# Kernel tuning notes

Hardware: AMD Instinct MI355X
Metric: run time of the kernel (lower is better)

## Reference

```python
import jax, jax.numpy as jnp
import numpy as np

B, S, D, H = 2, 2048, 1024, 16
DH = D // H  # 64


def setup_inputs() -> dict:
    key = jax.random.key(0)
    k1, k2, k3, k4 = jax.random.split(key, 4)
    x = jax.random.normal(k1, (B, S, D), dtype=jnp.float32)
    # causal mask: 0 => masked (matches mask==0 -> -inf in source)
    mask = jnp.tril(jnp.ones((S, S), dtype=jnp.int32))
    Wq = jax.random.normal(k2, (H, D, DH), dtype=jnp.float32) * (D ** -0.5)
    Wk = jax.random.normal(k3, (H, D, DH), dtype=jnp.float32) * (D ** -0.5)
    Wo = jax.random.normal(k4, (D, D), dtype=jnp.float32) * (D ** -0.5)
    bo = jnp.zeros((D,), dtype=jnp.float32)
    return {"x": x, "mask": mask, "Wq": Wq, "Wk": Wk, "Wo": Wo, "bo": bo}


def reference(x, mask, Wq, Wk, Wo, bo):
    # Per source: q = query(x), k = key(x), v = query(x)  (bug kept: v == q)
    q = jnp.einsum('bsd,hde->bhse', x, Wq)   # [B,H,S,DH]
    k = jnp.einsum('bsd,hde->bhse', x, Wk)   # [B,H,S,DH]
    # scale uses d_model (input dim), not d_head -- faithful to source
    scale = jnp.asarray(D, x.dtype) ** -0.5
    scores = jnp.einsum('bhse,bhte->bhst', q, k) * scale  # [B,H,S,S]
    neg_inf = jnp.asarray(float('-inf'), scores.dtype)
    scores = jnp.where(mask[None, None, :, :] == 0, neg_inf, scores)
    w = jax.nn.softmax(scores, axis=-1)
    attn = jnp.einsum('bhst,bhte->bhse', w, q)  # v == q
    # concat heads: head axis becomes contiguous feature blocks
    attn = attn.transpose(0, 2, 1, 3).reshape(B, S, D)
    return attn @ Wo + bo
```

## Files before the change

### kernel.cpp

```cpp
#include <hip/hip_runtime.h>
#include <hip/hip_bf16.h>

#define BQ 2
#define SQ 2048
#define DMODEL 1024
#define NH 16
#define DH 64
#define NQT (SQ / 64)

typedef __attribute__((ext_vector_type(8))) short bf16x8;
typedef __attribute__((ext_vector_type(4))) short bf16x4;
typedef __attribute__((ext_vector_type(4))) float f32x4;
typedef unsigned short u16;

__device__ __forceinline__ u16 f2b(float f) {
  __hip_bfloat16 h = __float2bfloat16(f);
  return *reinterpret_cast<u16*>(&h);
}

#define MFMA(a, b, c) __builtin_amdgcn_mfma_f32_16x16x32_bf16((a), (b), (c), 0, 0, 0)

__device__ __forceinline__ f32x4 mfma16(bf16x4 a, bf16x4 b, f32x4 c) {
  asm("v_mfma_f32_16x16x16_bf16 %0, %1, %2, %0" : "+v"(c) : "v"(a), "v"(b));
  return c;
}

__device__ __forceinline__ unsigned cvtpk(float lo, float hi) {
  unsigned r;
  asm("v_cvt_pk_bf16_f32 %0, %1, %2" : "=v"(r) : "v"(lo), "v"(hi));
  return r;
}

#define CS (0.03125f * 1.44269504088896f)


__global__ void cvt_x_kernel(const float* __restrict__ x, u16* __restrict__ xb, int n) {
  int i = blockIdx.x * blockDim.x + threadIdx.x;
  int stride = gridDim.x * blockDim.x;
  for (; i < n; i += stride) xb[i] = f2b(x[i]);
}

__global__ void transpose_head_kernel(const float* __restrict__ W, u16* __restrict__ WT) {
  int i = blockIdx.x * blockDim.x + threadIdx.x;
  const int total = NH * DMODEL * DH;
  int stride = gridDim.x * blockDim.x;
  for (; i < total; i += stride) {
    int h = i >> 16;
    int rem = i & 65535;
    int e = rem >> 10;
    int d = rem & 1023;
    WT[i] = f2b(W[((size_t)(h << 10) + d) * DH + e]);
  }
}

__global__ void transpose_wo_kernel(const float* __restrict__ Wo, u16* __restrict__ WoT) {
  int i = blockIdx.x * blockDim.x + threadIdx.x;
  const int total = DMODEL * DMODEL;
  int stride = gridDim.x * blockDim.x;
  for (; i < total; i += stride) {
    int nn = i >> 10, kk = i & 1023;
    WoT[i] = f2b(Wo[(size_t)kk * DMODEL + nn]);
  }
}

__global__ __launch_bounds__(256) void transpose_q_kernel(
    const u16* __restrict__ Q, u16* __restrict__ QT) {
  __shared__ alignas(16) u16 T[64][72];
  int st = blockIdx.x, h = blockIdx.y, b = blockIdx.z;
  size_t hb = ((size_t)(b * NH + h)) * SQ * DH;
  int tid = threadIdx.x;
#pragma unroll
  for (int i2 = 0; i2 < 2; ++i2) {
    int c = tid + i2 * 256;
    int r = c >> 3, cc = (c & 7) * 8;
    *(uint4*)&T[r][cc] = *(const uint4*)&Q[hb + (size_t)(st * 64 + r) * DH + cc];
  }
  __syncthreads();
#pragma unroll
  for (int i2 = 0; i2 < 2; ++i2) {
    int c = tid + i2 * 256;
    int e = c >> 3, s8 = (c & 7) * 8;
    u16 tmp[8];
#pragma unroll
    for (int j = 0; j < 8; ++j) tmp[j] = T[s8 + j][e];
    *(uint4*)&QT[hb + (size_t)e * SQ + st * 64 + s8] = *(uint4*)tmp;
  }
}


__global__ __launch_bounds__(256) void proj_kernel(
    const u16* __restrict__ xb,
    const u16* __restrict__ Wcat,
    u16* __restrict__ Qb, u16* __restrict__ Kb) {
  __shared__ alignas(16) u16 Xs[64][72];
  __shared__ alignas(16) u16 Ws[64][72];
  int st = blockIdx.x, hy = blockIdx.y, b = blockIdx.z;
  int tid = threadIdx.x;
  int w = tid >> 6, l = tid & 63;
  int lr = l & 15, lk = (l >> 4) * 8;
  f32x4 acc[4] = {};
  const u16* Ab = xb + (size_t)(b * SQ + st * 64) * DMODEL;
  const u16* Wb = Wcat + (size_t)hy * DH * DMODEL;
  for (int k0 = 0; k0 < DMODEL; k0 += 64) {
#pragma unroll
    for (int i2 = 0; i2 < 2; ++i2) {
      int c = tid + i2 * 256;
      int r = c >> 3, cc = (c & 7) * 8;
      *(uint4*)&Xs[r][cc] = *(const uint4*)&Ab[(size_t)r * DMODEL + k0 + cc];
      *(uint4*)&Ws[r][cc] = *(const uint4*)&Wb[(size_t)r * DMODEL + k0 + cc];
    }
    __syncthreads();
#pragma unroll
    for (int kk = 0; kk < 2; ++kk) {
      bf16x8 a = *(const bf16x8*)&Xs[w * 16 + lr][kk * 32 + lk];
#pragma unroll
      for (int n = 0; n < 4; ++n) {
        bf16x8 bb = *(const bf16x8*)&Ws[n * 16 + lr][kk * 32 + lk];
        acc[n] = MFMA(a, bb, acc[n]);
      }
    }
    __syncthreads();
  }
  bool isQ = (hy < NH);
  u16* dst = isQ ? Qb : Kb;
  float scale = isQ ? 1.0f : CS;
  int hh = hy & (NH - 1);
  size_t obase = ((size_t)(b * NH + hh) * SQ + st * 64) * DH;
  int r0 = w * 16 + ((l >> 4) << 2);
#pragma unroll
  for (int n = 0; n < 4; ++n)
#pragma unroll
    for (int r = 0; r < 4; ++r)
      dst[obase + (size_t)(r0 + r) * DH + n * 16 + lr] = f2b(acc[n][r] * scale);
}


__global__ __launch_bounds__(512) void attn_kernel(
    const u16* __restrict__ Qt,
    const u16* __restrict__ Kt,
    const u16* __restrict__ QTt,
    u16* __restrict__ Oc) {
  __shared__ alignas(16) u16 Ks[2][64][72];
  __shared__ alignas(16) u16 Vs[2][64][72];
  int bx = blockIdx.x, h = blockIdx.y, b = blockIdx.z;
  int p = b ? bx : (15 - bx);
  int tid = threadIdx.x, w = tid >> 6, l = tid & 63;
  int lr = l & 15, hi = l >> 4, lk = hi * 8;
  int qtile = 2 * p + (w >> 2);
  int q0 = qtile * 64 + (w & 3) * 16;
  int jmax = 2 * p + 1;
  size_t hb = ((size_t)(b * NH + h)) * SQ * DH;

  int r0s = tid >> 3, cc0 = (tid & 7) * 8;

  bf16x8 aq[2];
  {
    const u16* qrow = Qt + hb + (size_t)(q0 + lr) * DH;
    aq[0] = *(const bf16x8*)&qrow[lk];
    aq[1] = *(const bf16x8*)&qrow[32 + lk];
  }

  *(uint4*)&Ks[0][r0s][cc0] = *(const uint4*)&Kt[hb + (size_t)r0s * DH + cc0];
  *(uint4*)&Vs[0][r0s][cc0] = *(const uint4*)&QTt[hb + (size_t)r0s * SQ + cc0];
  __syncthreads();

  uint4 kreg = *(const uint4*)&Kt[hb + (size_t)(64 + r0s) * DH + cc0];
  uint4 vreg = *(const uint4*)&QTt[hb + (size_t)r0s * SQ + 64 + cc0];

  f32x4 acc_t[4] = {};
  float l_run = 0.f;
  int cur = 0;

  for (int j = 0; j <= jmax; ++j) {
    if (j <= qtile) {
      f32x4 s[4] = {};
#pragma unroll
      for (int kk = 0; kk < 2; ++kk)
#pragma unroll
        for (int n = 0; n < 4; ++n) {
          bf16x8 bk = *(const bf16x8*)&Ks[cur][n * 16 + lr][kk * 32 + lk];
          s[n] = MFMA(bk, aq[kk], s[n]);
        }

      if (j == qtile) {
        int qg = q0 + lr;
#pragma unroll
        for (int n = 0; n < 4; ++n) {
          int kbase = j * 64 + n * 16 + hi * 4;
#pragma unroll
          for (int r = 0; r < 4; ++r)
            s[n][r] = (kbase + r > qg) ? 0.f : exp2f(s[n][r]);
        }
      } else {
#pragma unroll
        for (int n = 0; n < 4; ++n)
#pragma unroll
          for (int r = 0; r < 4; ++r) s[n][r] = exp2f(s[n][r]);
      }

#pragma unroll
      for (int n = 0; n < 4; ++n)
        l_run += (s[n][0] + s[n][1]) + (s[n][2] + s[n][3]);

      bf16x4 pb[4];
#pragma unroll
      for (int n = 0; n < 4; ++n) {
        uint2 u;
        u.x = cvtpk(s[n][0], s[n][1]);
        u.y = cvtpk(s[n][2], s[n][3]);
        pb[n] = *(bf16x4*)&u;
      }

#pragma unroll
      for (int nv = 0; nv < 4; ++nv) {
        const u16* vrow = &Vs[cur][nv * 16 + lr][hi * 4];
#pragma unroll
        for (int nh = 0; nh < 4; ++nh) {
          bf16x4 va = *(const bf16x4*)&vrow[nh * 16];
          acc_t[nv] = mfma16(va, pb[nh], acc_t[nv]);
        }
      }
    }

    if (j < jmax) {
      *(uint4*)&Ks[cur ^ 1][r0s][cc0] = kreg;
      *(uint4*)&Vs[cur ^ 1][r0s][cc0] = vreg;
      if (j + 2 <= jmax) {
        kreg = *(const uint4*)&Kt[hb + (size_t)((j + 2) * 64 + r0s) * DH + cc0];
        vreg = *(const uint4*)&QTt[hb + (size_t)r0s * SQ + (j + 2) * 64 + cc0];
      }
      __syncthreads();
      cur ^= 1;
    }
  }

  l_run += __shfl_xor(l_run, 16, 64);
  l_run += __shfl_xor(l_run, 32, 64);
  float inv = 1.f / l_run;

  size_t rbase = ((size_t)b * SQ + q0 + lr) * DMODEL + h * DH;
#pragma unroll
  for (int nv = 0; nv < 4; ++nv) {
#pragma unroll
    for (int rp = 0; rp < 2; ++rp) {
      unsigned pw = cvtpk(acc_t[nv][2 * rp] * inv, acc_t[nv][2 * rp + 1] * inv);
      *(unsigned*)&Oc[rbase + nv * 16 + hi * 4 + 2 * rp] = pw;
    }
  }
}


__global__ __launch_bounds__(256) void outproj_kernel(
    const u16* __restrict__ Oc,
    const u16* __restrict__ WoT,
    const float* __restrict__ bo,
    float* __restrict__ out) {
  __shared__ alignas(16) u16 Xs[64][72];
  __shared__ alignas(16) u16 Ws[64][72];
  int rt = blockIdx.x, nt = blockIdx.y;
  int tid = threadIdx.x, w = tid >> 6, l = tid & 63;
  int lr = l & 15, lk = (l >> 4) * 8;
  f32x4 acc[4] = {};
  const u16* Ab = Oc + (size_t)rt * 64 * DMODEL;
  const u16* Wb = WoT + (size_t)nt * 64 * DMODEL;
  for (int k0 = 0; k0 < DMODEL; k0 += 64) {
#pragma unroll
    for (int i2 = 0; i2 < 2; ++i2) {
      int c = tid + i2 * 256;
      int r = c >> 3, cc = (c & 7) * 8;
      *(uint4*)&Xs[r][cc] = *(const uint4*)&Ab[(size_t)r * DMODEL + k0 + cc];
      *(uint4*)&Ws[r][cc] = *(const uint4*)&Wb[(size_t)r * DMODEL + k0 + cc];
    }
    __syncthreads();
#pragma unroll
    for (int kk = 0; kk < 2; ++kk) {
      bf16x8 a = *(const bf16x8*)&Xs[w * 16 + lr][kk * 32 + lk];
#pragma unroll
      for (int n = 0; n < 4; ++n) {
        bf16x8 bb = *(const bf16x8*)&Ws[n * 16 + lr][kk * 32 + lk];
        acc[n] = MFMA(a, bb, acc[n]);
      }
    }
    __syncthreads();
  }
  int r0 = w * 16 + ((l >> 4) << 2);
#pragma unroll
  for (int n = 0; n < 4; ++n) {
    int col = nt * 64 + n * 16 + lr;
    float bv = bo[col];
#pragma unroll
    for (int r = 0; r < 4; ++r)
      out[(size_t)(rt * 64 + r0 + r) * DMODEL + col] = acc[n][r] + bv;
  }
}


extern "C" void kernel_launch(void* const* d_in, const int* in_sizes, int n_in,
                              void* d_out, int out_size, void* d_ws, size_t ws_size,
                              hipStream_t stream) {
  const float* x  = (const float*)d_in[0];
  const float* Wq = (const float*)d_in[2];
  const float* Wk = (const float*)d_in[3];
  const float* Wo = (const float*)d_in[4];
  const float* bo = (const float*)d_in[5];
  float* out = (float*)d_out;

  char* ws = (char*)d_ws;
  u16* xb  = (u16*)ws;
  u16* WqT = xb + (size_t)BQ * SQ * DMODEL;
  u16* WkT = WqT + (size_t)NH * DH * DMODEL;
  u16* WoT = WkT + (size_t)NH * DH * DMODEL;
  u16* Qb  = WoT + (size_t)DMODEL * DMODEL;
  u16* Kb  = Qb + (size_t)BQ * NH * SQ * DH;
  u16* Ob  = Kb + (size_t)BQ * NH * SQ * DH;
  u16* QTb = xb;

  cvt_x_kernel<<<2048, 256, 0, stream>>>(x, xb, BQ * SQ * DMODEL);
  transpose_head_kernel<<<2048, 256, 0, stream>>>(Wq, WqT);
  transpose_head_kernel<<<2048, 256, 0, stream>>>(Wk, WkT);
  transpose_wo_kernel<<<1024, 256, 0, stream>>>(Wo, WoT);

  proj_kernel<<<dim3(SQ / 64, 2 * NH, BQ), 256, 0, stream>>>(xb, WqT, Qb, Kb);
  transpose_q_kernel<<<dim3(SQ / 64, NH, BQ), 256, 0, stream>>>(Qb, QTb);
  attn_kernel<<<dim3(16, NH, BQ), 512, 0, stream>>>(Qb, Kb, QTb, Ob);
  outproj_kernel<<<dim3(BQ * SQ / 64, DMODEL / 64, 1), 256, 0, stream>>>(Ob, WoT, bo, out);
}
```

Before: 130.0 us.

## Fuse weight transposes via LDS tiles, prefetch GEMM tiles, rebalance causal attention pairing

Replaces three strided scalar weight-transpose kernels with one tiled kernel that reads float4 rows and transposes through shared memory, so both reads and writes are coalesced. The projection and output GEMMs now load the next K-tile into registers while the current tile is consumed, overlapping global loads with MFMA work. The attention kernel now pairs query tile i with tile 31-i instead of using adjacent tile pairs, which evens out causal work across blocks. The attention loop bound is changed to match the new pairing, which must stay consistent with the unseen loop body.

```diff
diff --git a/kernel.cpp b/kernel.cpp
--- a/kernel.cpp
+++ b/kernel.cpp
@@ -18,6 +18,10 @@
   return *reinterpret_cast<u16*>(&h);
 }
 
+__device__ __forceinline__ unsigned packbf(float lo, float hi) {
+  return ((unsigned)f2b(hi) << 16) | (unsigned)f2b(lo);
+}
+
 #define MFMA(a, b, c) __builtin_amdgcn_mfma_f32_16x16x32_bf16((a), (b), (c), 0, 0, 0)
 
 __device__ __forceinline__ f32x4 mfma16(bf16x4 a, bf16x4 b, f32x4 c) {
@@ -40,26 +44,55 @@
   for (; i < n; i += stride) xb[i] = f2b(x[i]);
 }
 
-__global__ void transpose_head_kernel(const float* __restrict__ W, u16* __restrict__ WT) {
-  int i = blockIdx.x * blockDim.x + threadIdx.x;
-  const int total = NH * DMODEL * DH;
-  int stride = gridDim.x * blockDim.x;
-  for (; i < total; i += stride) {
-    int h = i >> 16;
-    int rem = i & 65535;
-    int e = rem >> 10;
-    int d = rem & 1023;
-    WT[i] = f2b(W[((size_t)(h << 10) + d) * DH + e]);
-  }
-}
-
-__global__ void transpose_wo_kernel(const float* __restrict__ Wo, u16* __restrict__ WoT) {
-  int i = blockIdx.x * blockDim.x + threadIdx.x;
-  const int total = DMODEL * DMODEL;
-  int stride = gridDim.x * blockDim.x;
-  for (; i < total; i += stride) {
-    int nn = i >> 10, kk = i & 1023;
-    WoT[i] = f2b(Wo[(size_t)kk * DMODEL + nn]);
+__global__ __launch_bounds__(256) void prep_w_kernel(
+    const float* __restrict__ Wq, const float* __restrict__ Wk,
+    const float* __restrict__ Wo,
+    u16* __restrict__ WqT, u16* __restrict__ WkT, u16* __restrict__ WoT) {
+  __shared__ alignas(16) u16 T[64][72];
+  int xt = blockIdx.x, yt = blockIdx.y, z = blockIdx.z;
+  int tid = threadIdx.x;
+  if (z < 2) {
+    const float* W = z ? Wk : Wq;
+    u16* WT = z ? WkT : WqT;
+    const float* src = W + ((size_t)yt * 1024 + xt * 64) * 64;
+#pragma unroll
+    for (int i = 0; i < 4; ++i) {
+      int lin = tid + i * 256;
+      int r = lin >> 4, c4 = (lin & 15) * 4;
+      float4 v = *(const float4*)&src[(size_t)r * 64 + c4];
+      *(unsigned*)&T[r][c4]     = packbf(v.x, v.y);
+      *(unsigned*)&T[r][c4 + 2] = packbf(v.z, v.w);
+    }
+    __syncthreads();
+#pragma unroll
+    for (int i = 0; i < 2; ++i) {
+      int lin = tid + i * 256;
+      int e = lin >> 3, d8 = (lin & 7) * 8;
+      u16 tmp[8];
+#pragma unroll
+      for (int j = 0; j < 8; ++j) tmp[j] = T[d8 + j][e];
+      *(uint4*)&WT[((size_t)yt * 64 + e) * 1024 + xt * 64 + d8] = *(uint4*)tmp;
+    }
+  } else {
+    const float* src = Wo + ((size_t)xt * 64) * 1024 + yt * 64;
+#pragma unroll
+    for (int i = 0; i < 4; ++i) {
+      int lin = tid + i * 256;
+      int r = lin >> 4, c4 = (lin & 15) * 4;
+      float4 v = *(const float4*)&src[(size_t)r * 1024 + c4];
+      *(unsigned*)&T[r][c4]     = packbf(v.x, v.y);
+      *(unsigned*)&T[r][c4 + 2] = packbf(v.z, v.w);
+    }
+    __syncthreads();
+#pragma unroll
+    for (int i = 0; i < 2; ++i) {
+      int lin = tid + i * 256;
+      int n = lin >> 3, k8 = (lin & 7) * 8;
+      u16 tmp[8];
+#pragma unroll
+      for (int j = 0; j < 8; ++j) tmp[j] = T[k8 + j][n];
+      *(uint4*)&WoT[((size_t)yt * 64 + n) * 1024 + xt * 64 + k8] = *(uint4*)tmp;
+    }
   }
 }
 
@@ -95,21 +128,25 @@
   __shared__ alignas(16) u16 Xs[64][72];
   __shared__ alignas(16) u16 Ws[64][72];
   int st = blockIdx.x, hy = blockIdx.y, b = blockIdx.z;
-  int tid = threadIdx.x;
-  int w = tid >> 6, l = tid & 63;
+  int tid = threadIdx.x, w = tid >> 6, l = tid & 63;
   int lr = l & 15, lk = (l >> 4) * 8;
+  int r0s = tid >> 3, cc0 = (tid & 7) * 8, r1s = r0s + 32;
   f32x4 acc[4] = {};
   const u16* Ab = xb + (size_t)(b * SQ + st * 64) * DMODEL;
   const u16* Wb = Wcat + (size_t)hy * DH * DMODEL;
-  for (int k0 = 0; k0 < DMODEL; k0 += 64) {
-#pragma unroll
-    for (int i2 = 0; i2 < 2; ++i2) {
-      int c = tid + i2 * 256;
-      int r = c >> 3, cc = (c & 7) * 8;
-      *(uint4*)&Xs[r][cc] = *(const uint4*)&Ab[(size_t)r * DMODEL + k0 + cc];
-      *(uint4*)&Ws[r][cc] = *(const uint4*)&Wb[(size_t)r * DMODEL + k0 + cc];
-    }
-    __syncthreads();
+
+  *(uint4*)&Xs[r0s][cc0] = *(const uint4*)&Ab[(size_t)r0s * DMODEL + cc0];
+  *(uint4*)&Xs[r1s][cc0] = *(const uint4*)&Ab[(size_t)r1s * DMODEL + cc0];
+  *(uint4*)&Ws[r0s][cc0] = *(const uint4*)&Wb[(size_t)r0s * DMODEL + cc0];
+  *(uint4*)&Ws[r1s][cc0] = *(const uint4*)&Wb[(size_t)r1s * DMODEL + cc0];
+  __syncthreads();
+
+  uint4 xr0 = *(const uint4*)&Ab[(size_t)r0s * DMODEL + 64 + cc0];
+  uint4 xr1 = *(const uint4*)&Ab[(size_t)r1s * DMODEL + 64 + cc0];
+  uint4 wv0 = *(const uint4*)&Wb[(size_t)r0s * DMODEL + 64 + cc0];
+  uint4 wv1 = *(const uint4*)&Wb[(size_t)r1s * DMODEL + 64 + cc0];
+
+  for (int ks = 0; ks < 16; ++ks) {
 #pragma unroll
     for (int kk = 0; kk < 2; ++kk) {
       bf16x8 a = *(const bf16x8*)&Xs[w * 16 + lr][kk * 32 + lk];
@@ -119,8 +156,23 @@
         acc[n] = MFMA(a, bb, acc[n]);
       }
     }
-    __syncthreads();
-  }
+    if (ks < 15) {
+      __syncthreads();
+      *(uint4*)&Xs[r0s][cc0] = xr0;
+      *(uint4*)&Xs[r1s][cc0] = xr1;
+      *(uint4*)&Ws[r0s][cc0] = wv0;
+      *(uint4*)&Ws[r1s][cc0] = wv1;
+      if (ks + 2 < 16) {
+        int k0 = (ks + 2) * 64;
+        xr0 = *(const uint4*)&Ab[(size_t)r0s * DMODEL + k0 + cc0];
+        xr1 = *(const uint4*)&Ab[(size_t)r1s * DMODEL + k0 + cc0];
+        wv0 = *(const uint4*)&Wb[(size_t)r0s * DMODEL + k0 + cc0];
+        wv1 = *(const uint4*)&Wb[(size_t)r1s * DMODEL + k0 + cc0];
+      }
+      __syncthreads();
+    }
+  }
+
   bool isQ = (hy < NH);
   u16* dst = isQ ? Qb : Kb;
   float scale = isQ ? 1.0f : CS;
@@ -143,12 +195,12 @@
   __shared__ alignas(16) u16 Ks[2][64][72];
   __shared__ alignas(16) u16 Vs[2][64][72];
   int bx = blockIdx.x, h = blockIdx.y, b = blockIdx.z;
-  int p = b ? bx : (15 - bx);
   int tid = threadIdx.x, w = tid >> 6, l = tid & 63;
   int lr = l & 15, hi = l >> 4, lk = hi * 8;
-  int qtile = 2 * p + (w >> 2);
+  int qlo = bx, qhi = NQT - 1 - bx;
+  int qtile = (w >> 2) ? qhi : qlo;
   int q0 = qtile * 64 + (w & 3) * 16;
-  int jmax = 2 * p + 1;
+  int jmax = qhi;
   size_t hb = ((size_t)(b * NH + h)) * SQ * DH;
 
   int r0s = tid >> 3, cc0 = (tid & 7) * 8;
@@ -260,18 +312,23 @@
   int rt = blockIdx.x, nt = blockIdx.y;
   int tid = threadIdx.x, w = tid >> 6, l = tid & 63;
   int lr = l & 15, lk = (l >> 4) * 8;
+  int r0s = tid >> 3, cc0 = (tid & 7) * 8, r1s = r0s + 32;
   f32x4 acc[4] = {};
   const u16* Ab = Oc + (size_t)rt * 64 * DMODEL;
   const u16* Wb = WoT + (size_t)nt * 64 * DMODEL;
-  for (int k0 = 0; k0 < DMODEL; k0 += 64) {
-#pragma unroll
-    for (int i2 = 0; i2 < 2; ++i2) {
-      int c = tid + i2 * 256;
-      int r = c >> 3, cc = (c & 7) * 8;
-      *(uint4*)&Xs[r][cc] = *(const uint4*)&Ab[(size_t)r * DMODEL + k0 + cc];
-      *(uint4*)&Ws[r][cc] = *(const uint4*)&Wb[(size_t)r * DMODEL + k0 + cc];
-    }
-    __syncthreads();
+
+  *(uint4*)&Xs[r0s][cc0] = *(const uint4*)&Ab[(size_t)r0s * DMODEL + cc0];
+  *(uint4*)&Xs[r1s][cc0] = *(const uint4*)&Ab[(size_t)r1s * DMODEL + cc0];
+  *(uint4*)&Ws[r0s][cc0] = *(const uint4*)&Wb[(size_t)r0s * DMODEL + cc0];
+  *(uint4*)&Ws[r1s][cc0] = *(const uint4*)&Wb[(size_t)r1s * DMODEL + cc0];
+  __syncthreads();
+
+  uint4 xr0 = *(const uint4*)&Ab[(size_t)r0s * DMODEL + 64 + cc0];
+  uint4 xr1 = *(const uint4*)&Ab[(size_t)r1s * DMODEL + 64 + cc0];
+  uint4 wv0 = *(const uint4*)&Wb[(size_t)r0s * DMODEL + 64 + cc0];
+  uint4 wv1 = *(const uint4*)&Wb[(size_t)r1s * DMODEL + 64 + cc0];
+
+  for (int ks = 0; ks < 16; ++ks) {
 #pragma unroll
     for (int kk = 0; kk < 2; ++kk) {
       bf16x8 a = *(const bf16x8*)&Xs[w * 16 + lr][kk * 32 + lk];
@@ -281,8 +338,23 @@
         acc[n] = MFMA(a, bb, acc[n]);
       }
     }
-    __syncthreads();
-  }
+    if (ks < 15) {
+      __syncthreads();
+      *(uint4*)&Xs[r0s][cc0] = xr0;
+      *(uint4*)&Xs[r1s][cc0] = xr1;
+      *(uint4*)&Ws[r0s][cc0] = wv0;
+      *(uint4*)&Ws[r1s][cc0] = wv1;
+      if (ks + 2 < 16) {
+        int k0 = (ks + 2) * 64;
+        xr0 = *(const uint4*)&Ab[(size_t)r0s * DMODEL + k0 + cc0];
+        xr1 = *(const uint4*)&Ab[(size_t)r1s * DMODEL + k0 + cc0];
+        wv0 = *(const uint4*)&Wb[(size_t)r0s * DMODEL + k0 + cc0];
+        wv1 = *(const uint4*)&Wb[(size_t)r1s * DMODEL + k0 + cc0];
+      }
+      __syncthreads();
+    }
+  }
+
   int r0 = w * 16 + ((l >> 4) << 2);
 #pragma unroll
   for (int n = 0; n < 4; ++n) {
@@ -316,9 +388,7 @@
   u16* QTb = xb;
 
   cvt_x_kernel<<<2048, 256, 0, stream>>>(x, xb, BQ * SQ * DMODEL);
-  transpose_head_kernel<<<2048, 256, 0, stream>>>(Wq, WqT);
-  transpose_head_kernel<<<2048, 256, 0, stream>>>(Wk, WkT);
-  transpose_wo_kernel<<<1024, 256, 0, stream>>>(Wo, WoT);
+  prep_w_kernel<<<dim3(16, 16, 3), 256, 0, stream>>>(Wq, Wk, Wo, WqT, WkT, WoT);
 
   proj_kernel<<<dim3(SQ / 64, 2 * NH, BQ), 256, 0, stream>>>(xb, WqT, Qb, Kb);
   transpose_q_kernel<<<dim3(SQ / 64, NH, BQ), 256, 0, stream>>>(Qb, QTb);
```

Measured after the change: 116.2 us. 1.12x faster.
